# Optimization experiments

Measured on AMD Instinct MI355X. Metric: run time of the kernel, lower is better.

Reference implementation:

```python
import itertools
import jax, jax.numpy as jnp
import numpy as np

B, RES, RES_, STRIDE = 512, 14, 7, 2
IN_DIM, OUT_DIM, KEY_DIM, H, ATTN_RATIO = 256, 512, 16, 8, 2
NH_KD = KEY_DIM * H          # 128
D = ATTN_RATIO * KEY_DIM     # 32
DH = D * H                   # 256
KV_OUT = DH + NH_KD          # 384
N, N_ = RES * RES, RES_ * RES_   # 196, 49
EPS = 1e-5
SCALE = KEY_DIM ** -0.5


def _build_bias_idxs():
    points = list(itertools.product(range(RES), range(RES)))
    points_ = list(itertools.product(range(RES_), range(RES_)))
    offsets, idxs = {}, []
    for p1 in points_:
        for p2 in points:
            off = (abs(p1[0] * STRIDE - p2[0]), abs(p1[1] * STRIDE - p2[1]))
            if off not in offsets:
                offsets[off] = len(offsets)
            idxs.append(offsets[off])
    return np.array(idxs, dtype=np.int32).reshape(N_, N), len(offsets)


def _bn(x, g, b, m, v):
    # inference-mode BatchNorm1d over last dim
    return (x - m) * (g * jax.lax.rsqrt(v + EPS)) + b


def _hardswish(x):
    return x * jnp.clip(x + 3.0, 0.0, 6.0) * (1.0 / 6.0)


def setup_inputs() -> dict:
    key = jax.random.key(0)
    ks = jax.random.split(key, 16)
    idxs_np, n_off = _build_bias_idxs()
    inp = {
        "x": jax.random.normal(ks[0], (B, N, IN_DIM), jnp.float32),
        "w_kv": jax.random.normal(ks[1], (KV_OUT, IN_DIM), jnp.float32) * 0.02,
        "kv_g": jnp.ones((KV_OUT,), jnp.float32),
        "kv_b": jax.random.normal(ks[2], (KV_OUT,), jnp.float32) * 0.01,
        "kv_m": jax.random.normal(ks[3], (KV_OUT,), jnp.float32) * 0.01,
        "kv_v": jax.random.uniform(ks[4], (KV_OUT,), jnp.float32) + 0.5,
        "w_q": jax.random.normal(ks[5], (NH_KD, IN_DIM), jnp.float32) * 0.02,
        "q_g": jnp.ones((NH_KD,), jnp.float32),
        "q_b": jax.random.normal(ks[6], (NH_KD,), jnp.float32) * 0.01,
        "q_m": jax.random.normal(ks[7], (NH_KD,), jnp.float32) * 0.01,
        "q_v": jax.random.uniform(ks[8], (NH_KD,), jnp.float32) + 0.5,
        "w_p": jax.random.normal(ks[9], (OUT_DIM, DH), jnp.float32) * 0.02,
        "p_g": jnp.ones((OUT_DIM,), jnp.float32),
        "p_b": jax.random.normal(ks[10], (OUT_DIM,), jnp.float32) * 0.01,
        "p_m": jax.random.normal(ks[11], (OUT_DIM,), jnp.float32) * 0.01,
        "p_v": jax.random.uniform(ks[12], (OUT_DIM,), jnp.float32) + 0.5,
        "ab_table": jax.random.normal(ks[13], (H, n_off), jnp.float32) * 0.02,
        "bias_idxs": jnp.asarray(idxs_np),  # [N_, N] int32
    }
    return inp


def reference(x, w_kv, kv_g, kv_b, kv_m, kv_v,
              w_q, q_g, q_b, q_m, q_v,
              w_p, p_g, p_b, p_m, p_v,
              ab_table, bias_idxs):
    Bx = x.shape[0]
    # kv projection: [B, N, KV_OUT] -> split heads into k [B,H,N,KEY_DIM], v [B,H,N,D]
    kv = _bn(jnp.einsum('bnc,oc->bno', x, w_kv), kv_g, kv_b, kv_m, kv_v)
    kv = kv.reshape(Bx, N, H, KEY_DIM + D)
    k = kv[..., :KEY_DIM].transpose(0, 2, 1, 3)   # [B,H,N,KEY_DIM]
    v = kv[..., KEY_DIM:].transpose(0, 2, 1, 3)   # [B,H,N,D]
    # query path: spatial subsample then Linear+BN
    xs = x.reshape(Bx, RES, RES, IN_DIM)[:, ::STRIDE, ::STRIDE].reshape(Bx, N_, IN_DIM)
    q = _bn(jnp.einsum('bnc,oc->bno', xs, w_q), q_g, q_b, q_m, q_v)
    q = q.reshape(Bx, N_, H, KEY_DIM).transpose(0, 2, 1, 3)  # [B,H,N_,KEY_DIM]
    # relative-position bias gather: [H, N_, N]
    ab = ab_table[:, bias_idxs]
    attn = jnp.einsum('bhqd,bhkd->bhqk', q, k) * SCALE + ab
    attn = jax.nn.softmax(attn, axis=-1)
    out = jnp.einsum('bhqk,bhkd->bhqd', attn, v)           # [B,H,N_,D]
    out = out.transpose(0, 2, 1, 3).reshape(Bx, N_, DH)
    out = _hardswish(out)
    out = _bn(jnp.einsum('bnd,od->bno', out, w_p), p_g, p_b, p_m, p_v)
    return out
```

## Files before the change

kernel.cpp:

```cpp
#include <hip/hip_runtime.h>

typedef __attribute__((ext_vector_type(8))) short bf16x8;
typedef __attribute__((ext_vector_type(4))) float f32x4;
typedef __attribute__((ext_vector_type(4))) short short4v;
typedef __attribute__((ext_vector_type(4))) unsigned int u32x4;
typedef __attribute__((ext_vector_type(2))) unsigned int u32x2;

#define DEVFN static __device__ __forceinline__

DEVFN short f2bf(float f) {
  unsigned int u = __builtin_bit_cast(unsigned int, f);
  unsigned int r = (u + 0x7FFFu + ((u >> 16) & 1u)) >> 16;
  return (short)r;
}

DEVFN unsigned int pack2bf(float a, float b) {
  unsigned int lo = (unsigned int)(unsigned short)f2bf(a);
  unsigned int hi = (unsigned int)(unsigned short)f2bf(b);
  return lo | (hi << 16);
}

DEVFN f32x4 mfma_bf16(bf16x8 a, bf16x8 b, f32x4 c) {
  return __builtin_amdgcn_mfma_f32_16x16x32_bf16(a, b, c, 0, 0, 0);
}

DEVFN f32x4 zero4() { f32x4 z = {0.f, 0.f, 0.f, 0.f}; return z; }
DEVFN bf16x8 zero8() { bf16x8 z = {0,0,0,0,0,0,0,0}; return z; }

DEVFN void gload_lds16(const void* g, void* l) {
  __builtin_amdgcn_global_load_lds(
      (const __attribute__((address_space(1))) unsigned int*)g,
      (__attribute__((address_space(3))) unsigned int*)l, 16, 0, 0);
}

DEVFN bf16x8 lds8(const short* p) {
  short4v lo = *reinterpret_cast<const short4v*>(p);
  short4v hi = *reinterpret_cast<const short4v*>(p + 4);
  bf16x8 r;
  r[0] = lo[0]; r[1] = lo[1]; r[2] = lo[2]; r[3] = lo[3];
  r[4] = hi[0]; r[5] = hi[1]; r[6] = hi[2]; r[7] = hi[3];
  return r;
}

DEVFN bf16x8 cvt8v(float4 u0, float4 u1) {
  bf16x8 r;
  r[0] = f2bf(u0.x); r[1] = f2bf(u0.y); r[2] = f2bf(u0.z); r[3] = f2bf(u0.w);
  r[4] = f2bf(u1.x); r[5] = f2bf(u1.y); r[6] = f2bf(u1.z); r[7] = f2bf(u1.w);
  return r;
}

DEVFN float bfhi2f(unsigned int hi16) {
  return __builtin_bit_cast(float, hi16 << 16);
}
DEVFN float bfhi2f_hi(unsigned int word) {
  return __builtin_bit_cast(float, word & 0xffff0000u);
}

__global__ void pack_w_k(const float* __restrict__ w, const float* __restrict__ g,
                         const float* __restrict__ b, const float* __restrict__ m,
                         const float* __restrict__ v, short* __restrict__ pk,
                         float* __restrict__ bias, int O) {
  const int t = blockIdx.x * 256 + threadIdx.x;
  const int nt = O >> 4;
  const int total = nt * 8 * 64;
  if (t < total) {
    int lane = t & 63;
    int j = (t >> 6) % nt;
    int c = (t >> 6) / nt;
    int row = j * 16 + (lane & 15);
    int col = c * 32 + (lane >> 4) * 8;
    float s = g[row] * rsqrtf(v[row] + 1e-5f);
    const float* wp = w + (size_t)row * 256 + col;
    short* o = pk + (size_t)t * 8;
#pragma unroll
    for (int e = 0; e < 8; ++e) o[e] = f2bf(wp[e] * s);
  }
  if (t < O) {
    float s = g[t] * rsqrtf(v[t] + 1e-5f);
    bias[t] = b[t] - m[t] * s;
  }
}

__global__ void ab_gather2(const float* __restrict__ tab,
                           const int* __restrict__ idxs,
                           u32x2* __restrict__ ab3, int n_off) {
  const int blk = blockIdx.x;
  const int t = blk % 13, w = (blk / 13) & 3, h = blk / 52;
  const int lane = threadIdx.x;
  const int l15 = lane & 15, g = lane >> 4;
  int q = w * 16 + l15; if (q > 48) q = 48;
  const int nb = (t >> 1) * 32 + g * 8 + (t & 1) * 4;
  u32x2 out; out[0] = 0u; out[1] = 0u;
  if (nb < 196) {
    const int* irow = idxs + q * 196 + nb;
    const float* th = tab + h * n_off;
    out[0] = pack2bf(th[irow[0]], th[irow[1]]);
    out[1] = pack2bf(th[irow[2]], th[irow[3]]);
  }
  ab3[(size_t)blk * 64 + lane] = out;
}

__global__ void kv_gemm5(
    const float* __restrict__ x, const short* __restrict__ pk,
    const float* __restrict__ bias, short* __restrict__ k_out,
    short* __restrict__ vT_out) {
  __shared__ short xs2[16384];
  const int tid = threadIdx.x, w = tid >> 6, lane = tid & 63;
  const int l15 = lane & 15, g = lane >> 4;
  const int mt = blockIdx.x;

  const float* xb = x + (size_t)mt * 64 * 256;
#pragma unroll
  for (int it = 0; it < 4; ++it) {
    int i = it * 512 + tid;
    int row = i >> 5, gc = i & 31;
    const float* src = xb + row * 256 + gc * 8;
    float4 u0 = *reinterpret_cast<const float4*>(src);
    float4 u1 = *reinterpret_cast<const float4*>(src + 4);
    *reinterpret_cast<bf16x8*>(reinterpret_cast<char*>(xs2) + row * 512 +
                               ((gc * 16) ^ ((row & 7) << 4))) = cvt8v(u0, u1);
  }
  __syncthreads();

  f32x4 acc[4][3];
#pragma unroll
  for (int m = 0; m < 4; ++m) {
    acc[m][0] = zero4(); acc[m][1] = zero4(); acc[m][2] = zero4();
  }
  const int swz = (l15 & 7) << 4;
#pragma unroll
  for (int c = 0; c < 8; ++c) {
    bf16x8 wf0 = *reinterpret_cast<const bf16x8*>(pk + ((size_t)(c * 24 + 3 * w) * 64 + lane) * 8);
    bf16x8 wf1 = *reinterpret_cast<const bf16x8*>(pk + ((size_t)(c * 24 + 3 * w + 1) * 64 + lane) * 8);
    bf16x8 wf2 = *reinterpret_cast<const bf16x8*>(pk + ((size_t)(c * 24 + 3 * w + 2) * 64 + lane) * 8);
#pragma unroll
    for (int m = 0; m < 4; ++m) {
      const int row = m * 16 + l15;
      bf16x8 a = *reinterpret_cast<const bf16x8*>(
          reinterpret_cast<const char*>(xs2) + row * 512 +
          ((c * 64 + g * 16) ^ swz));
      acc[m][0] = mfma_bf16(a, wf0, acc[m][0]);
      acc[m][1] = mfma_bf16(a, wf1, acc[m][1]);
      acc[m][2] = mfma_bf16(a, wf2, acc[m][2]);
    }
  }

  const float bvK = bias[(3 * w) * 16 + l15];
  const float bv1 = bias[(3 * w + 1) * 16 + l15];
  const float bv2 = bias[(3 * w + 2) * 16 + l15];
#pragma unroll
  for (int m = 0; m < 4; ++m) {
    const int row0 = mt * 64 + m * 16 + g * 4;
    const int bb_ = row0 / 196, n0 = row0 % 196;
    short* kp = k_out + ((size_t)(bb_ * 8 + w) * 196 + n0) * 16 + l15;
#pragma unroll
    for (int r = 0; r < 4; ++r) kp[r * 16] = f2bf(acc[m][0][r] + bvK);
    short4v sv;
#pragma unroll
    for (int r = 0; r < 4; ++r) sv[r] = f2bf(acc[m][1][r] + bv1);
    *reinterpret_cast<short4v*>(
        vT_out + ((size_t)(bb_ * 8 + w) * 32 + l15) * 196 + n0) = sv;
#pragma unroll
    for (int r = 0; r < 4; ++r) sv[r] = f2bf(acc[m][2][r] + bv2);
    *reinterpret_cast<short4v*>(
        vT_out + ((size_t)(bb_ * 8 + w) * 32 + 16 + l15) * 196 + n0) = sv;
  }
}

__global__ __launch_bounds__(256) void q_gemm2(
    const float* __restrict__ x, const short* __restrict__ pk,
    const float* __restrict__ bias, short* __restrict__ out) {
  __shared__ short bs[8 * 512];
  __shared__ float sb[128];
  const int tid = threadIdx.x, w_id = tid >> 6, lane = tid & 63;
  const int l15 = lane & 15, gq = lane >> 4;
  const int mt = blockIdx.x;
  if (tid < 128) sb[tid] = bias[tid];
  const int arow = mt * 64 + w_id * 16 + l15;
  const int b = arow / 49, qi = arow % 49;
  const int n = 28 * (qi / 7) + 2 * (qi % 7);
  const float* xrow = x + ((size_t)b * 196 + n) * 256;

  f32x4 acc[8];
#pragma unroll
  for (int j = 0; j < 8; ++j) acc[j] = zero4();

  for (int c = 0; c < 8; ++c) {
    for (int seg = w_id; seg < 8; seg += 4)
      gload_lds16(pk + ((size_t)(c * 8 + seg) * 64 + lane) * 8, &bs[seg * 512]);
    const float4 u0 = *reinterpret_cast<const float4*>(xrow + c * 32 + gq * 8);
    const float4 u1 = *reinterpret_cast<const float4*>(xrow + c * 32 + gq * 8 + 4);
    bf16x8 a = cvt8v(u0, u1);
    __syncthreads();
#pragma unroll
    for (int j = 0; j < 8; ++j) {
      bf16x8 bj = *reinterpret_cast<const bf16x8*>(&bs[(j * 64 + lane) * 8]);
      acc[j] = mfma_bf16(a, bj, acc[j]);
    }
    __syncthreads();
  }
  const int orow = mt * 64 + w_id * 16 + gq * 4;
#pragma unroll
  for (int j = 0; j < 8; ++j) {
    int ch = j * 16 + l15;
    float bb = sb[ch];
#pragma unroll
    for (int r = 0; r < 4; ++r)
      out[(size_t)(orow + r) * 128 + ch] = f2bf(acc[j][r] + bb);
  }
}

__global__ __launch_bounds__(256) void attn4_k(
    const short* __restrict__ k_ws, const short* __restrict__ vT_ws,
    const short* __restrict__ qw, const u32x2* __restrict__ ab3,
    short* __restrict__ out) {
  __shared__ short vt[6304];
  __shared__ short kst[3200];
  const int b = blockIdx.x >> 3, h = blockIdx.x & 7;
  const int tid = threadIdx.x, w_id = tid >> 6, lane = tid & 63;
  const int l15 = lane & 15, g = lane >> 4;

  if (tid < 16) *reinterpret_cast<unsigned int*>(&vt[6272 + tid * 2]) = 0u;

  const short* vsrc = vT_ws + (size_t)(b * 8 + h) * 6272;
  for (int s = w_id; s < 13; s += 4) {
    if (s * 64 + lane < 784)
      gload_lds16(vsrc + (size_t)(s * 64 + lane) * 8, &vt[s * 512]);
  }
  const short* ksrc = k_ws + (size_t)(b * 8 + h) * 3136;
  for (int s = w_id; s < 7; s += 4) {
    if (s * 64 + lane < 392)
      gload_lds16(ksrc + (size_t)(s * 64 + lane) * 8, &kst[s * 512]);
  }

  const int q = w_id * 16 + l15;
  const bool qok = q < 49;
  bf16x8 bq = zero8();
  if (g < 2 && qok)
    bq = *reinterpret_cast<const bf16x8*>(
        qw + ((size_t)b * 49 + q) * 128 + h * 16 + g * 8);

  __syncthreads();

  f32x4 s[13];
#pragma unroll
  for (int t = 0; t < 13; ++t) {
    int n_a = (t >> 1) * 32 + (l15 >> 2) * 8 + (t & 1) * 4 + (l15 & 3);
    bf16x8 ak = zero8();
    if (g < 2 && n_a < 196) ak = lds8(&kst[n_a * 16 + g * 8]);
    s[t] = mfma_bf16(ak, bq, zero4());
  }

  const u32x2* abp = ab3 + (size_t)((h * 4 + w_id) * 13) * 64 + lane;
#pragma unroll
  for (int t = 0; t < 13; ++t) {
    int nb = (t >> 1) * 32 + g * 8 + (t & 1) * 4;
    if (nb < 196) {
      u32x2 bv = abp[t * 64];
      s[t][0] = s[t][0] * 0.25f + bfhi2f(bv[0]);
      s[t][1] = s[t][1] * 0.25f + bfhi2f_hi(bv[0]);
      s[t][2] = s[t][2] * 0.25f + bfhi2f(bv[1]);
      s[t][3] = s[t][3] * 0.25f + bfhi2f_hi(bv[1]);
    } else {
      s[t][0] = -1e30f; s[t][1] = -1e30f; s[t][2] = -1e30f; s[t][3] = -1e30f;
    }
  }

  float mx = s[0][0];
#pragma unroll
  for (int t = 0; t < 13; ++t)
    mx = fmaxf(mx, fmaxf(fmaxf(s[t][0], s[t][1]), fmaxf(s[t][2], s[t][3])));
  mx = fmaxf(mx, __shfl_xor(mx, 16, 64));
  mx = fmaxf(mx, __shfl_xor(mx, 32, 64));
  float sum = 0.f;
#pragma unroll
  for (int t = 0; t < 13; ++t) {
#pragma unroll
    for (int r = 0; r < 4; ++r) {
      float e = __expf(s[t][r] - mx);
      s[t][r] = e;
      sum += e;
    }
  }
  sum += __shfl_xor(sum, 16, 64);
  sum += __shfl_xor(sum, 32, 64);
  const float inv = 1.f / sum;

  unsigned int pkr[14][2];
#pragma unroll
  for (int t = 0; t < 13; ++t) {
    pkr[t][0] = pack2bf(s[t][0] * inv, s[t][1] * inv);
    pkr[t][1] = pack2bf(s[t][2] * inv, s[t][3] * inv);
  }
  pkr[13][0] = 0u; pkr[13][1] = 0u;

  f32x4 o0 = zero4(), o1 = zero4();
#pragma unroll
  for (int c = 0; c < 7; ++c) {
    u32x4 bp_u;
    bp_u[0] = pkr[2 * c][0];     bp_u[1] = pkr[2 * c][1];
    bp_u[2] = pkr[2 * c + 1][0]; bp_u[3] = pkr[2 * c + 1][1];
    bf16x8 bp = __builtin_bit_cast(bf16x8, bp_u);
    bf16x8 a0 = lds8(&vt[l15 * 196 + c * 32 + g * 8]);
    bf16x8 a1 = lds8(&vt[(16 + l15) * 196 + c * 32 + g * 8]);
    o0 = mfma_bf16(a0, bp, o0);
    o1 = mfma_bf16(a1, bp, o1);
  }

  if (qok) {
    short* op = out + (((size_t)b * 49 + q) * 256 + h * 32 + g * 4);
    short4v v0, v1;
#pragma unroll
    for (int r = 0; r < 4; ++r) {
      float x0 = o0[r];
      v0[r] = f2bf(x0 * fminf(fmaxf(x0 + 3.f, 0.f), 6.f) * (1.f / 6.f));
      float x1 = o1[r];
      v1[r] = f2bf(x1 * fminf(fmaxf(x1 + 3.f, 0.f), 6.f) * (1.f / 6.f));
    }
    *reinterpret_cast<short4v*>(op) = v0;
    *reinterpret_cast<short4v*>(op + 16) = v1;
  }
}

__global__ void p_gemm3(
    const short* __restrict__ a_in, const short* __restrict__ pk,
    const float* __restrict__ bias, float* __restrict__ out) {
  __shared__ short as_[32 * 256];
  const int tid = threadIdx.x, w = tid >> 6, lane = tid & 63;
  const int l15 = lane & 15, g = lane >> 4;
  const int half = blockIdx.x & 1;
  const int mt = blockIdx.x >> 1;

  const short* ab_ = a_in + (size_t)mt * 32 * 256;
#pragma unroll
  for (int it = 0; it < 4; ++it) {
    int i = it * 256 + tid;
    int row = i >> 5, gc = i & 31;
    bf16x8 vv = *reinterpret_cast<const bf16x8*>(ab_ + row * 256 + gc * 8);
    *reinterpret_cast<bf16x8*>(reinterpret_cast<char*>(as_) + row * 512 +
                               ((gc * 16) ^ ((row & 7) << 4))) = vv;
  }
  __syncthreads();

  f32x4 acc[2][4];
#pragma unroll
  for (int m = 0; m < 2; ++m)
#pragma unroll
    for (int jj = 0; jj < 4; ++jj) acc[m][jj] = zero4();

  const int jbase = half * 16 + w * 4;
#pragma unroll
  for (int c = 0; c < 8; ++c) {
    bf16x8 wf[4];
#pragma unroll
    for (int jj = 0; jj < 4; ++jj)
      wf[jj] = *reinterpret_cast<const bf16x8*>(
          pk + ((size_t)(c * 32 + jbase + jj) * 64 + lane) * 8);
#pragma unroll
    for (int m = 0; m < 2; ++m) {
      const int row = m * 16 + l15;
      bf16x8 a = *reinterpret_cast<const bf16x8*>(
          reinterpret_cast<const char*>(as_) + row * 512 +
          ((c * 64 + g * 16) ^ ((row & 7) << 4)));
#pragma unroll
      for (int jj = 0; jj < 4; ++jj)
        acc[m][jj] = mfma_bf16(a, wf[jj], acc[m][jj]);
    }
  }

#pragma unroll
  for (int m = 0; m < 2; ++m) {
    const int row0 = mt * 32 + m * 16 + g * 4;
#pragma unroll
    for (int jj = 0; jj < 4; ++jj) {
      const int och = (jbase + jj) * 16 + l15;
      const float bv = bias[och];
#pragma unroll
      for (int r = 0; r < 4; ++r)
        out[(size_t)(row0 + r) * 512 + och] = acc[m][jj][r] + bv;
    }
  }
}

extern "C" void kernel_launch(void* const* d_in, const int* in_sizes, int n_in,
                              void* d_out, int out_size, void* d_ws, size_t ws_size,
                              hipStream_t stream) {
  const float* x    = (const float*)d_in[0];
  const float* w_kv = (const float*)d_in[1];
  const float* kv_g = (const float*)d_in[2];
  const float* kv_b = (const float*)d_in[3];
  const float* kv_m = (const float*)d_in[4];
  const float* kv_v = (const float*)d_in[5];
  const float* w_q  = (const float*)d_in[6];
  const float* q_g  = (const float*)d_in[7];
  const float* q_b  = (const float*)d_in[8];
  const float* q_m  = (const float*)d_in[9];
  const float* q_v  = (const float*)d_in[10];
  const float* w_p  = (const float*)d_in[11];
  const float* p_g  = (const float*)d_in[12];
  const float* p_b  = (const float*)d_in[13];
  const float* p_m  = (const float*)d_in[14];
  const float* p_v  = (const float*)d_in[15];
  const float* ab_t = (const float*)d_in[16];
  const int*   idxs = (const int*)d_in[17];
  const int n_off = in_sizes[16] / 8;

  char* ws = (char*)d_ws;
  short* pk_kv  = (short*)(ws);
  short* pk_q   = (short*)(ws + 196608);
  short* pk_p   = (short*)(ws + 262144);
  float* bs_kv  = (float*)(ws + 524288);
  float* bs_q   = (float*)(ws + 525824);
  float* bs_p   = (float*)(ws + 526336);
  u32x2* ab3_ws = (u32x2*)(ws + 528384);
  short* k_ws   = (short*)(ws + 835712);
  short* vT_ws  = (short*)(ws + 26525824);
  short* q_ws   = (short*)(ws + 77906048);
  short* at_ws  = (short*)(ws + 84328576);

  pack_w_k<<<dim3(48), dim3(256), 0, stream>>>(w_kv, kv_g, kv_b, kv_m, kv_v, pk_kv, bs_kv, 384);
  pack_w_k<<<dim3(16), dim3(256), 0, stream>>>(w_q, q_g, q_b, q_m, q_v, pk_q, bs_q, 128);
  pack_w_k<<<dim3(64), dim3(256), 0, stream>>>(w_p, p_g, p_b, p_m, p_v, pk_p, bs_p, 512);
  ab_gather2<<<dim3(416), dim3(64), 0, stream>>>(ab_t, idxs, ab3_ws, n_off);

  kv_gemm5<<<dim3(1568), dim3(512), 0, stream>>>(x, pk_kv, bs_kv, k_ws, vT_ws);
  q_gemm2<<<dim3(392), dim3(256), 0, stream>>>(x, pk_q, bs_q, q_ws);
  attn4_k<<<dim3(4096), dim3(256), 0, stream>>>(k_ws, vT_ws, q_ws, ab3_ws, at_ws);
  p_gemm3<<<dim3(1568), dim3(256), 0, stream>>>(at_ws, pk_p, bs_p, (float*)d_out);
}
```

Measured before the change: 130.8 us.

## Merge prologue kernels and fuse kv and q GEMMs into one launch

The three weight-pack kernels and the bias gather are merged into one prologue kernel that dispatches on block index. The kv and q projection GEMMs are merged into a single 512-thread launch, with q blocks now each covering 128 rows using 8 waves. This cuts the launch count from six to two before attention and lets q work fill the tail of the kv grid. In exchange, the merged kernel carries a larger shared allocation, plus a launch_bounds of 512 threads with a minimum of 4 blocks per CU, which may constrain register allocation.

```diff
diff --git a/kernel.cpp b/kernel.cpp
--- a/kernel.cpp
+++ b/kernel.cpp
@@ -56,11 +56,10 @@
   return __builtin_bit_cast(float, word & 0xffff0000u);
 }
 
-__global__ void pack_w_k(const float* __restrict__ w, const float* __restrict__ g,
-                         const float* __restrict__ b, const float* __restrict__ m,
-                         const float* __restrict__ v, short* __restrict__ pk,
-                         float* __restrict__ bias, int O) {
-  const int t = blockIdx.x * 256 + threadIdx.x;
+DEVFN void pack_w_body(const float* __restrict__ w, const float* __restrict__ g,
+                       const float* __restrict__ b, const float* __restrict__ m,
+                       const float* __restrict__ v, short* __restrict__ pk,
+                       float* __restrict__ bias, int O, int t) {
   const int nt = O >> 4;
   const int total = nt * 8 * 64;
   if (t < total) {
@@ -81,132 +80,153 @@
   }
 }
 
-__global__ void ab_gather2(const float* __restrict__ tab,
-                           const int* __restrict__ idxs,
-                           u32x2* __restrict__ ab3, int n_off) {
-  const int blk = blockIdx.x;
-  const int t = blk % 13, w = (blk / 13) & 3, h = blk / 52;
-  const int lane = threadIdx.x;
-  const int l15 = lane & 15, g = lane >> 4;
-  int q = w * 16 + l15; if (q > 48) q = 48;
-  const int nb = (t >> 1) * 32 + g * 8 + (t & 1) * 4;
-  u32x2 out; out[0] = 0u; out[1] = 0u;
-  if (nb < 196) {
-    const int* irow = idxs + q * 196 + nb;
-    const float* th = tab + h * n_off;
-    out[0] = pack2bf(th[irow[0]], th[irow[1]]);
-    out[1] = pack2bf(th[irow[2]], th[irow[3]]);
-  }
-  ab3[(size_t)blk * 64 + lane] = out;
-}
-
-__global__ void kv_gemm5(
-    const float* __restrict__ x, const short* __restrict__ pk,
-    const float* __restrict__ bias, short* __restrict__ k_out,
-    short* __restrict__ vT_out) {
-  __shared__ short xs2[16384];
+__global__ __launch_bounds__(256) void prologue_k(
+    const float* __restrict__ w_kv, const float* __restrict__ kv_g,
+    const float* __restrict__ kv_b, const float* __restrict__ kv_m,
+    const float* __restrict__ kv_v, short* __restrict__ pk_kv,
+    float* __restrict__ bs_kv,
+    const float* __restrict__ w_q, const float* __restrict__ q_g,
+    const float* __restrict__ q_b, const float* __restrict__ q_m,
+    const float* __restrict__ q_v, short* __restrict__ pk_q,
+    float* __restrict__ bs_q,
+    const float* __restrict__ w_p, const float* __restrict__ p_g,
+    const float* __restrict__ p_b, const float* __restrict__ p_m,
+    const float* __restrict__ p_v, short* __restrict__ pk_p,
+    float* __restrict__ bs_p,
+    const float* __restrict__ tab, const int* __restrict__ idxs,
+    u32x2* __restrict__ ab3, int n_off) {
+  const int blk = blockIdx.x, tid = threadIdx.x;
+  if (blk < 48) {
+    pack_w_body(w_kv, kv_g, kv_b, kv_m, kv_v, pk_kv, bs_kv, 384, blk * 256 + tid);
+  } else if (blk < 64) {
+    pack_w_body(w_q, q_g, q_b, q_m, q_v, pk_q, bs_q, 128, (blk - 48) * 256 + tid);
+  } else if (blk < 128) {
+    pack_w_body(w_p, p_g, p_b, p_m, p_v, pk_p, bs_p, 512, (blk - 64) * 256 + tid);
+  } else {
+    const int vb = (blk - 128) * 4 + (tid >> 6);
+    const int lane = tid & 63;
+    if (vb < 416) {
+      const int t = vb % 13, w = (vb / 13) & 3, h = vb / 52;
+      const int l15 = lane & 15, g = lane >> 4;
+      int q = w * 16 + l15; if (q > 48) q = 48;
+      const int nb = (t >> 1) * 32 + g * 8 + (t & 1) * 4;
+      u32x2 out; out[0] = 0u; out[1] = 0u;
+      if (nb < 196) {
+        const int* irow = idxs + q * 196 + nb;
+        const float* th = tab + h * n_off;
+        out[0] = pack2bf(th[irow[0]], th[irow[1]]);
+        out[1] = pack2bf(th[irow[2]], th[irow[3]]);
+      }
+      ab3[(size_t)vb * 64 + lane] = out;
+    }
+  }
+}
+
+__global__ __launch_bounds__(512, 4) void kvq_k(
+    const float* __restrict__ x,
+    const short* __restrict__ pk_kv, const float* __restrict__ bs_kv,
+    short* __restrict__ k_out, short* __restrict__ vT_out,
+    const short* __restrict__ pk_q, const float* __restrict__ bs_q,
+    short* __restrict__ q_out) {
+  __shared__ short smem[16640];
   const int tid = threadIdx.x, w = tid >> 6, lane = tid & 63;
   const int l15 = lane & 15, g = lane >> 4;
-  const int mt = blockIdx.x;
-
-  const float* xb = x + (size_t)mt * 64 * 256;
-#pragma unroll
-  for (int it = 0; it < 4; ++it) {
-    int i = it * 512 + tid;
-    int row = i >> 5, gc = i & 31;
-    const float* src = xb + row * 256 + gc * 8;
-    float4 u0 = *reinterpret_cast<const float4*>(src);
-    float4 u1 = *reinterpret_cast<const float4*>(src + 4);
-    *reinterpret_cast<bf16x8*>(reinterpret_cast<char*>(xs2) + row * 512 +
-                               ((gc * 16) ^ ((row & 7) << 4))) = cvt8v(u0, u1);
-  }
-  __syncthreads();
-
-  f32x4 acc[4][3];
-#pragma unroll
-  for (int m = 0; m < 4; ++m) {
-    acc[m][0] = zero4(); acc[m][1] = zero4(); acc[m][2] = zero4();
-  }
-  const int swz = (l15 & 7) << 4;
-#pragma unroll
-  for (int c = 0; c < 8; ++c) {
-    bf16x8 wf0 = *reinterpret_cast<const bf16x8*>(pk + ((size_t)(c * 24 + 3 * w) * 64 + lane) * 8);
-    bf16x8 wf1 = *reinterpret_cast<const bf16x8*>(pk + ((size_t)(c * 24 + 3 * w + 1) * 64 + lane) * 8);
-    bf16x8 wf2 = *reinterpret_cast<const bf16x8*>(pk + ((size_t)(c * 24 + 3 * w + 2) * 64 + lane) * 8);
+
+  if (blockIdx.x < 1568) {
+    short* xs2 = smem;
+    const int mt = blockIdx.x;
+    const float* xb = x + (size_t)mt * 64 * 256;
+#pragma unroll
+    for (int it = 0; it < 4; ++it) {
+      int i = it * 512 + tid;
+      int row = i >> 5, gc = i & 31;
+      const float* src = xb + row * 256 + gc * 8;
+      float4 u0 = *reinterpret_cast<const float4*>(src);
+      float4 u1 = *reinterpret_cast<const float4*>(src + 4);
+      *reinterpret_cast<bf16x8*>(reinterpret_cast<char*>(xs2) + row * 512 +
+                                 ((gc * 16) ^ ((row & 7) << 4))) = cvt8v(u0, u1);
+    }
+    __syncthreads();
+
+    f32x4 acc[4][3];
 #pragma unroll
     for (int m = 0; m < 4; ++m) {
-      const int row = m * 16 + l15;
-      bf16x8 a = *reinterpret_cast<const bf16x8*>(
-          reinterpret_cast<const char*>(xs2) + row * 512 +
-          ((c * 64 + g * 16) ^ swz));
-      acc[m][0] = mfma_bf16(a, wf0, acc[m][0]);
-      acc[m][1] = mfma_bf16(a, wf1, acc[m][1]);
-      acc[m][2] = mfma_bf16(a, wf2, acc[m][2]);
-    }
-  }
-
-  const float bvK = bias[(3 * w) * 16 + l15];
-  const float bv1 = bias[(3 * w + 1) * 16 + l15];
-  const float bv2 = bias[(3 * w + 2) * 16 + l15];
-#pragma unroll
-  for (int m = 0; m < 4; ++m) {
-    const int row0 = mt * 64 + m * 16 + g * 4;
-    const int bb_ = row0 / 196, n0 = row0 % 196;
-    short* kp = k_out + ((size_t)(bb_ * 8 + w) * 196 + n0) * 16 + l15;
-#pragma unroll
-    for (int r = 0; r < 4; ++r) kp[r * 16] = f2bf(acc[m][0][r] + bvK);
-    short4v sv;
-#pragma unroll
-    for (int r = 0; r < 4; ++r) sv[r] = f2bf(acc[m][1][r] + bv1);
-    *reinterpret_cast<short4v*>(
-        vT_out + ((size_t)(bb_ * 8 + w) * 32 + l15) * 196 + n0) = sv;
-#pragma unroll
-    for (int r = 0; r < 4; ++r) sv[r] = f2bf(acc[m][2][r] + bv2);
-    *reinterpret_cast<short4v*>(
-        vT_out + ((size_t)(bb_ * 8 + w) * 32 + 16 + l15) * 196 + n0) = sv;
-  }
-}
-
-__global__ __launch_bounds__(256) void q_gemm2(
-    const float* __restrict__ x, const short* __restrict__ pk,
-    const float* __restrict__ bias, short* __restrict__ out) {
-  __shared__ short bs[8 * 512];
-  __shared__ float sb[128];
-  const int tid = threadIdx.x, w_id = tid >> 6, lane = tid & 63;
-  const int l15 = lane & 15, gq = lane >> 4;
-  const int mt = blockIdx.x;
-  if (tid < 128) sb[tid] = bias[tid];
-  const int arow = mt * 64 + w_id * 16 + l15;
-  const int b = arow / 49, qi = arow % 49;
-  const int n = 28 * (qi / 7) + 2 * (qi % 7);
-  const float* xrow = x + ((size_t)b * 196 + n) * 256;
-
-  f32x4 acc[8];
-#pragma unroll
-  for (int j = 0; j < 8; ++j) acc[j] = zero4();
-
-  for (int c = 0; c < 8; ++c) {
-    for (int seg = w_id; seg < 8; seg += 4)
-      gload_lds16(pk + ((size_t)(c * 8 + seg) * 64 + lane) * 8, &bs[seg * 512]);
-    const float4 u0 = *reinterpret_cast<const float4*>(xrow + c * 32 + gq * 8);
-    const float4 u1 = *reinterpret_cast<const float4*>(xrow + c * 32 + gq * 8 + 4);
-    bf16x8 a = cvt8v(u0, u1);
-    __syncthreads();
+      acc[m][0] = zero4(); acc[m][1] = zero4(); acc[m][2] = zero4();
+    }
+    const int swz = (l15 & 7) << 4;
+#pragma unroll
+    for (int c = 0; c < 8; ++c) {
+      bf16x8 wf0 = *reinterpret_cast<const bf16x8*>(pk_kv + ((size_t)(c * 24 + 3 * w) * 64 + lane) * 8);
+      bf16x8 wf1 = *reinterpret_cast<const bf16x8*>(pk_kv + ((size_t)(c * 24 + 3 * w + 1) * 64 + lane) * 8);
+      bf16x8 wf2 = *reinterpret_cast<const bf16x8*>(pk_kv + ((size_t)(c * 24 + 3 * w + 2) * 64 + lane) * 8);
+#pragma unroll
+      for (int m = 0; m < 4; ++m) {
+        const int row = m * 16 + l15;
+        bf16x8 a = *reinterpret_cast<const bf16x8*>(
+            reinterpret_cast<const char*>(xs2) + row * 512 +
+            ((c * 64 + g * 16) ^ swz));
+        acc[m][0] = mfma_bf16(a, wf0, acc[m][0]);
+        acc[m][1] = mfma_bf16(a, wf1, acc[m][1]);
+        acc[m][2] = mfma_bf16(a, wf2, acc[m][2]);
+      }
+    }
+
+    const float bvK = bs_kv[(3 * w) * 16 + l15];
+    const float bv1 = bs_kv[(3 * w + 1) * 16 + l15];
+    const float bv2 = bs_kv[(3 * w + 2) * 16 + l15];
+#pragma unroll
+    for (int m = 0; m < 4; ++m) {
+      const int row0 = mt * 64 + m * 16 + g * 4;
+      const int bb_ = row0 / 196, n0 = row0 % 196;
+      short* kp = k_out + ((size_t)(bb_ * 8 + w) * 196 + n0) * 16 + l15;
+#pragma unroll
+      for (int r = 0; r < 4; ++r) kp[r * 16] = f2bf(acc[m][0][r] + bvK);
+      short4v sv;
+#pragma unroll
+      for (int r = 0; r < 4; ++r) sv[r] = f2bf(acc[m][1][r] + bv1);
+      *reinterpret_cast<short4v*>(
+          vT_out + ((size_t)(bb_ * 8 + w) * 32 + l15) * 196 + n0) = sv;
+#pragma unroll
+      for (int r = 0; r < 4; ++r) sv[r] = f2bf(acc[m][2][r] + bv2);
+      *reinterpret_cast<short4v*>(
+          vT_out + ((size_t)(bb_ * 8 + w) * 32 + 16 + l15) * 196 + n0) = sv;
+    }
+  } else {
+    short* bs = smem;
+    float* sb = reinterpret_cast<float*>(smem + 4096);
+    const int mt = blockIdx.x - 1568;
+    if (tid < 128) sb[tid] = bs_q[tid];
+    const int arow = mt * 128 + w * 16 + l15;
+    const int b = arow / 49, qi = arow % 49;
+    const int n = 28 * (qi / 7) + 2 * (qi % 7);
+    const float* xrow = x + ((size_t)b * 196 + n) * 256;
+
+    f32x4 acc[8];
+#pragma unroll
+    for (int j = 0; j < 8; ++j) acc[j] = zero4();
+
+    for (int c = 0; c < 8; ++c) {
+      gload_lds16(pk_q + ((size_t)(c * 8 + w) * 64 + lane) * 8, &bs[w * 512]);
+      const float4 u0 = *reinterpret_cast<const float4*>(xrow + c * 32 + g * 8);
+      const float4 u1 = *reinterpret_cast<const float4*>(xrow + c * 32 + g * 8 + 4);
+      bf16x8 a = cvt8v(u0, u1);
+      __syncthreads();
+#pragma unroll
+      for (int j = 0; j < 8; ++j) {
+        bf16x8 bj = *reinterpret_cast<const bf16x8*>(&bs[(j * 64 + lane) * 8]);
+        acc[j] = mfma_bf16(a, bj, acc[j]);
+      }
+      __syncthreads();
+    }
+    const int orow = mt * 128 + w * 16 + g * 4;
 #pragma unroll
     for (int j = 0; j < 8; ++j) {
-      bf16x8 bj = *reinterpret_cast<const bf16x8*>(&bs[(j * 64 + lane) * 8]);
-      acc[j] = mfma_bf16(a, bj, acc[j]);
-    }
-    __syncthreads();
-  }
-  const int orow = mt * 64 + w_id * 16 + gq * 4;
-#pragma unroll
-  for (int j = 0; j < 8; ++j) {
-    int ch = j * 16 + l15;
-    float bb = sb[ch];
-#pragma unroll
-    for (int r = 0; r < 4; ++r)
-      out[(size_t)(orow + r) * 128 + ch] = f2bf(acc[j][r] + bb);
+      int ch = j * 16 + l15;
+      float bb = sb[ch];
+#pragma unroll
+      for (int r = 0; r < 4; ++r)
+        q_out[(size_t)(orow + r) * 128 + ch] = f2bf(acc[j][r] + bb);
+    }
   }
 }
 
@@ -418,13 +438,14 @@
   short* q_ws   = (short*)(ws + 77906048);
   short* at_ws  = (short*)(ws + 84328576);
 
-  pack_w_k<<<dim3(48), dim3(256), 0, stream>>>(w_kv, kv_g, kv_b, kv_m, kv_v, pk_kv, bs_kv, 384);
-  pack_w_k<<<dim3(16), dim3(256), 0, stream>>>(w_q, q_g, q_b, q_m, q_v, pk_q, bs_q, 128);
-  pack_w_k<<<dim3(64), dim3(256), 0, stream>>>(w_p, p_g, p_b, p_m, p_v, pk_p, bs_p, 512);
-  ab_gather2<<<dim3(416), dim3(64), 0, stream>>>(ab_t, idxs, ab3_ws, n_off);
-
-  kv_gemm5<<<dim3(1568), dim3(512), 0, stream>>>(x, pk_kv, bs_kv, k_ws, vT_ws);
-  q_gemm2<<<dim3(392), dim3(256), 0, stream>>>(x, pk_q, bs_q, q_ws);
+  prologue_k<<<dim3(232), dim3(256), 0, stream>>>(
+      w_kv, kv_g, kv_b, kv_m, kv_v, pk_kv, bs_kv,
+      w_q, q_g, q_b, q_m, q_v, pk_q, bs_q,
+      w_p, p_g, p_b, p_m, p_v, pk_p, bs_p,
+      ab_t, idxs, ab3_ws, n_off);
+
+  kvq_k<<<dim3(1764), dim3(512), 0, stream>>>(
+      x, pk_kv, bs_kv, k_ws, vT_ws, pk_q, bs_q, q_ws);
   attn4_k<<<dim3(4096), dim3(256), 0, stream>>>(k_ws, vT_ws, q_ws, ab3_ws, at_ws);
   p_gemm3<<<dim3(1568), dim3(256), 0, stream>>>(at_ws, pk_p, bs_p, (float*)d_out);
 }
```

After: 114.7 us (median of 2 runs). -12.3%, faster.
